# Performance work log

Measured on AMD Instinct MI355X. Metric: run time of the kernel, lower is better.

The kernel has to match this reference:

```python
import jax, jax.numpy as jnp
import numpy as np

K = 16  # knn_graph k, loop=True (self included since d(i,i)=0 is minimal)


def _knn_idx(pos, k):
    # exact kNN via pairwise squared distances; [N, k] neighbor indices
    sq = jnp.sum(pos * pos, axis=-1)
    d2 = sq[:, None] + sq[None, :] - 2.0 * (pos @ pos.T)  # [N, N]
    _, idx = jax.lax.top_k(-d2, k)
    return idx


def _pointnet_conv(x, pos, idx, Wa, ba, Wb, bb):
    # PointNetConv: msg = MLP(concat(x_j, pos_j - pos_i)), max-aggregate over neighbors
    rel = pos[idx] - pos[:, None, :]                    # [N, K, 3]
    m = jnp.concatenate([x[idx], rel], axis=-1)          # [N, K, Cin+3]
    h = jax.nn.relu(m @ Wa + ba) @ Wb + bb               # [N, K, Cout]
    return jnp.max(h, axis=1)                            # [N, Cout]


def setup_inputs() -> dict:
    key = jax.random.key(0)
    ks = jax.random.split(key, 13)
    N = 8192
    c1, c2, c3 = 64, 64, 128
    s = lambda fi: 1.0 / np.sqrt(fi)
    pos = jax.random.normal(ks[0], (N, 3), dtype=jnp.float32)
    return {
        "pos": pos,
        "W1a": jax.random.normal(ks[1], (3 + 3, c1), jnp.float32) * s(6),
        "b1a": jnp.zeros((c1,), jnp.float32),
        "W1b": jax.random.normal(ks[2], (c1, c1), jnp.float32) * s(c1),
        "b1b": jnp.zeros((c1,), jnp.float32),
        "W2a": jax.random.normal(ks[3], (c1 + 3, c2), jnp.float32) * s(c1 + 3),
        "b2a": jnp.zeros((c2,), jnp.float32),
        "W2b": jax.random.normal(ks[4], (c2, c2), jnp.float32) * s(c2),
        "b2b": jnp.zeros((c2,), jnp.float32),
        "W3a": jax.random.normal(ks[5], (c2 + 3, c3), jnp.float32) * s(c2 + 3),
        "b3a": jnp.zeros((c3,), jnp.float32),
        "W3b": jax.random.normal(ks[6], (c3, c3), jnp.float32) * s(c3),
        "b3b": jnp.zeros((c3,), jnp.float32),
    }


def reference(pos, W1a, b1a, W1b, b1b, W2a, b2a, W2b, b2b, W3a, b3a, W3b, b3b):
    idx = _knn_idx(pos, K)
    h1 = jax.nn.relu(_pointnet_conv(pos, pos, idx, W1a, b1a, W1b, b1b))
    h2 = jax.nn.relu(_pointnet_conv(h1, pos, idx, W2a, b2a, W2b, b2b))
    h3 = jax.nn.relu(_pointnet_conv(h2, pos, idx, W3a, b3a, W3b, b3b))
    return (h1, h2, h3)
```

## Files before the change

### kernel.cpp

```cpp
#include <hip/hip_runtime.h>
#include <math.h>

#define N_PTS 8192
#define KNN 16

typedef __attribute__((ext_vector_type(8))) short bf16x8;
typedef __attribute__((ext_vector_type(4))) float f32x4v;

__device__ __forceinline__ unsigned short f2bf(float f)
{
    unsigned u = __float_as_uint(f);
    u = u + 0x7fffu + ((u >> 16) & 1u);
    return (unsigned short)(u >> 16);
}
__device__ __forceinline__ unsigned pack2(float a, float b)
{
    return (unsigned)f2bf(a) | ((unsigned)f2bf(b) << 16);
}
__device__ __forceinline__ float rfl(float x)
{
    return __int_as_float(__builtin_amdgcn_readfirstlane(__float_as_int(x)));
}

__global__ __launch_bounds__(256) void prep_all(
    const float* __restrict__ pos, float4* __restrict__ pos4,
    const float* __restrict__ w1a, const float* __restrict__ w1b,
    const float* __restrict__ w2a, const float* __restrict__ w2b,
    const float* __restrict__ w3a, const float* __restrict__ w3b,
    uint4* __restrict__ dst)
{
    const int b = blockIdx.x;
    if (b < 88) {
        if (threadIdx.x >= 64) return;
        const float* Ws[6] = {w1a, w1b, w2a, w2b, w3a, w3b};
        const int Kd[6] = {6, 64, 67, 64, 67, 128};
        const int Nd[6] = {64, 64, 64, 64, 128, 128};
        const int start[7] = {0, 4, 12, 24, 32, 56, 88};
        int m = 0;
        while (b >= start[m + 1]) ++m;
        const int f  = b - start[m];
        const int NT = Nd[m] / 16;
        const int ks = f / NT, nt = f % NT;
        const int lane = threadIdx.x;
        const int c  = nt * 16 + (lane & 15);
        const int k0 = ks * 32 + (lane >> 4) * 8;
        const int K = Kd[m], N = Nd[m];
        const float* W = Ws[m];
        float v[8];
#pragma unroll
        for (int j = 0; j < 8; ++j) {
            const int kk = k0 + j;
            v[j] = (kk < K) ? W[kk * N + c] : 0.0f;
        }
        uint4 o;
        o.x = pack2(v[0], v[1]); o.y = pack2(v[2], v[3]);
        o.z = pack2(v[4], v[5]); o.w = pack2(v[6], v[7]);
        dst[b * 64 + lane] = o;
    } else {
        const int i = (b - 88) * 256 + threadIdx.x;
        const float x = pos[i * 3 + 0];
        const float y = pos[i * 3 + 1];
        const float z = pos[i * 3 + 2];
        pos4[i] = make_float4(x, y, z, fmaf(x, x, fmaf(y, y, z * z)));
    }
}

__device__ __forceinline__ unsigned sortkey(const float d2)
{
    unsigned u = __float_as_uint(d2);
    u ^= (unsigned)((int)u >> 31) | 0x80000000u;
    return u;
}

constexpr int CAP = 128;
constexpr int QB  = 8;
constexpr int NWV = 8;

__global__ __launch_bounds__(512, 8) void knn_kernel(const float4* __restrict__ pos4,
                                                     int* __restrict__ idx_out)
{
    __shared__ float mins[QB][NWV][64];
    __shared__ float Ts[QB];
    __shared__ unsigned long long surv[QB][CAP];
    __shared__ int scnt[QB];

    const int tid   = threadIdx.x;
    const int w     = tid >> 6;
    const int lane  = tid & 63;
    const int qbase = blockIdx.x * QB;
    const int cbase = w * (N_PTS / NWV);

    if (tid < QB) scnt[tid] = 0;

    float qx[QB], qy[QB], qz[QB];
#pragma unroll
    for (int qi = 0; qi < QB; ++qi) {
        const float4 qp = pos4[qbase + qi];
        qx[qi] = rfl(-2.0f * qp.x);
        qy[qi] = rfl(-2.0f * qp.y);
        qz[qi] = rfl(-2.0f * qp.z);
    }

    float mn[QB];
#pragma unroll
    for (int qi = 0; qi < QB; ++qi) mn[qi] = 1e30f;

    const float4* cp = pos4 + cbase + lane;

    {
        float4 c0 = cp[0 * 64], c1 = cp[1 * 64], c2 = cp[2 * 64], c3 = cp[3 * 64];
#pragma unroll 1
        for (int t = 0; t < 12; t += 4) {
            const float4 n0 = cp[(t + 4) * 64];
            const float4 n1 = cp[(t + 5) * 64];
            const float4 n2 = cp[(t + 6) * 64];
            const float4 n3 = cp[(t + 7) * 64];
#pragma unroll
            for (int qi = 0; qi < QB; ++qi) {
                mn[qi] = fminf(mn[qi], fmaf(qx[qi], c0.x, fmaf(qy[qi], c0.y, fmaf(qz[qi], c0.z, c0.w))));
                mn[qi] = fminf(mn[qi], fmaf(qx[qi], c1.x, fmaf(qy[qi], c1.y, fmaf(qz[qi], c1.z, c1.w))));
                mn[qi] = fminf(mn[qi], fmaf(qx[qi], c2.x, fmaf(qy[qi], c2.y, fmaf(qz[qi], c2.z, c2.w))));
                mn[qi] = fminf(mn[qi], fmaf(qx[qi], c3.x, fmaf(qy[qi], c3.y, fmaf(qz[qi], c3.z, c3.w))));
            }
            c0 = n0; c1 = n1; c2 = n2; c3 = n3;
        }
#pragma unroll
        for (int qi = 0; qi < QB; ++qi) {
            mn[qi] = fminf(mn[qi], fmaf(qx[qi], c0.x, fmaf(qy[qi], c0.y, fmaf(qz[qi], c0.z, c0.w))));
            mn[qi] = fminf(mn[qi], fmaf(qx[qi], c1.x, fmaf(qy[qi], c1.y, fmaf(qz[qi], c1.z, c1.w))));
            mn[qi] = fminf(mn[qi], fmaf(qx[qi], c2.x, fmaf(qy[qi], c2.y, fmaf(qz[qi], c2.z, c2.w))));
            mn[qi] = fminf(mn[qi], fmaf(qx[qi], c3.x, fmaf(qy[qi], c3.y, fmaf(qz[qi], c3.z, c3.w))));
        }
    }
#pragma unroll
    for (int qi = 0; qi < QB; ++qi) mins[qi][w][lane] = mn[qi];
    __syncthreads();

    {
        const int q = w;
        float v = mins[q][0][lane];
#pragma unroll
        for (int k = 1; k < NWV; ++k) v = fminf(v, mins[q][k][lane]);
#pragma unroll
        for (int kk = 2; kk <= 64; kk <<= 1)
#pragma unroll
            for (int j = kk >> 1; j > 0; j >>= 1) {
                const float o = __shfl_xor(v, j);
                const bool up = ((lane & kk) == 0);
                const bool lo = ((lane & j) == 0);
                v = (up == lo) ? fminf(v, o) : fmaxf(v, o);
            }
        if (lane == 15) Ts[q] = v;
    }
    __syncthreads();

    float T[QB];
#pragma unroll
    for (int qi = 0; qi < QB; ++qi) T[qi] = rfl(Ts[qi]);

    {
        float4 c0 = cp[0 * 64], c1 = cp[1 * 64], c2 = cp[2 * 64], c3 = cp[3 * 64];
#pragma unroll 1
        for (int t = 0; t < 16; t += 4) {
            float4 n0, n1, n2, n3;
            if (t < 12) {
                n0 = cp[(t + 4) * 64]; n1 = cp[(t + 5) * 64];
                n2 = cp[(t + 6) * 64]; n3 = cp[(t + 7) * 64];
            }
#pragma unroll
            for (int u = 0; u < 4; ++u) {
                const float4 p = (u == 0) ? c0 : (u == 1) ? c1 : (u == 2) ? c2 : c3;
                const int j = cbase + (t + u) * 64 + lane;
#pragma unroll
                for (int qi = 0; qi < QB; ++qi) {
                    const float s = fmaf(qx[qi], p.x, fmaf(qy[qi], p.y, fmaf(qz[qi], p.z, p.w)));
                    if (s <= T[qi]) {
                        const int slot = atomicAdd(&scnt[qi], 1);
                        if (slot < CAP)
                            surv[qi][slot] = ((unsigned long long)sortkey(s) << 32) | (unsigned)j;
                    }
                }
            }
            if (t < 12) { c0 = n0; c1 = n1; c2 = n2; c3 = n3; }
        }
    }
    __syncthreads();

    {
        const int q = w;
        const int n = min(scnt[q], CAP);
        const unsigned long long k0 = (lane < n) ? surv[q][lane] : ~0ull;
        const unsigned long long k1 = (lane + 64 < n) ? surv[q][lane + 64] : ~0ull;
        int r0 = 0, r1 = 0;
#pragma unroll 4
        for (int e = 0; e < n; ++e) {
            const unsigned long long ke = surv[q][e];
            r0 += (ke < k0) ? 1 : 0;
            r1 += (ke < k1) ? 1 : 0;
        }
        if (lane < n && r0 < KNN)
            idx_out[(qbase + q) * KNN + r0] = (int)(unsigned)(k0 & 0xFFFFFFFFu);
        if (lane + 64 < n && r1 < KNN)
            idx_out[(qbase + q) * KNN + r1] = (int)(unsigned)(k1 & 0xFFFFFFFFu);
    }
}

template <int CIN, int CMID, int COUT, int WM, int WN>
__global__ __launch_bounds__(256) void conv_mfma(
    const float* __restrict__ x, const float* __restrict__ pos,
    const int* __restrict__ idx,
    const uint4* __restrict__ fA, const float* __restrict__ ba,
    const uint4* __restrict__ fB, const float* __restrict__ bb,
    float* __restrict__ out)
{
    constexpr int PB  = 8, M = 128;
    constexpr int K1  = (CIN + 3 + 31) & ~31;
    constexpr int KS1 = K1 / 32;
    constexpr int KP1 = K1 + 8;
    constexpr int KS2 = CMID / 32;
    constexpr int KP2 = CMID + 8;
    constexpr int NT  = COUT / 16;
    constexpr int NTW = NT / WN;
    constexpr int MFW = (M / 16) / WM;
    constexpr int MSGS = M * KP1;
    constexpr int HBS  = M * KP2;
    constexpr int BUFS = (MSGS > HBS) ? MSGS : HBS;

    __shared__ int nbr[M];
    __shared__ __align__(16) unsigned short buf[BUFS];

    const int tid  = threadIdx.x;
    const int lane = tid & 63;
    const int w    = tid >> 6;
    const int wm   = w / WN, wn = w % WN;
    const int i0   = blockIdx.x * PB;

    if (tid < M) nbr[tid] = idx[i0 * KNN + tid];
    __syncthreads();

    if constexpr (CIN == 3) {
        if (tid < M) {
            const int row = tid, p = row >> 4, j = nbr[row];
            const float ax = pos[j * 3 + 0], ay = pos[j * 3 + 1], az = pos[j * 3 + 2];
            const float bx = pos[(i0 + p) * 3 + 0], by = pos[(i0 + p) * 3 + 1],
                        bz = pos[(i0 + p) * 3 + 2];
            uint4 c0;
            c0.x = pack2(ax, ay);
            c0.y = pack2(az, ax - bx);
            c0.z = pack2(ay - by, az - bz);
            c0.w = 0u;
            *reinterpret_cast<uint4*>(&buf[row * KP1 + 0])  = c0;
            const uint4 z = make_uint4(0, 0, 0, 0);
            *reinterpret_cast<uint4*>(&buf[row * KP1 + 8])  = z;
            *reinterpret_cast<uint4*>(&buf[row * KP1 + 16]) = z;
            *reinterpret_cast<uint4*>(&buf[row * KP1 + 24]) = z;
        }
    } else {
        const int row = tid >> 1, hh = tid & 1;
        const int j = nbr[row];
        const float* xr = x + j * CIN + hh * 32;
#pragma unroll
        for (int cc = 0; cc < 32; cc += 8) {
            const float4 f0 = *reinterpret_cast<const float4*>(xr + cc);
            const float4 f1 = *reinterpret_cast<const float4*>(xr + cc + 4);
            uint4 o;
            o.x = pack2(f0.x, f0.y); o.y = pack2(f0.z, f0.w);
            o.z = pack2(f1.x, f1.y); o.w = pack2(f1.z, f1.w);
            *reinterpret_cast<uint4*>(&buf[row * KP1 + hh * 32 + cc]) = o;
        }
        if (hh) {
            const int p = row >> 4;
            const float rx = pos[j * 3 + 0] - pos[(i0 + p) * 3 + 0];
            const float ry = pos[j * 3 + 1] - pos[(i0 + p) * 3 + 1];
            const float rz = pos[j * 3 + 2] - pos[(i0 + p) * 3 + 2];
            uint4 c0;
            c0.x = pack2(rx, ry);
            c0.y = pack2(rz, 0.0f);
            c0.z = 0u; c0.w = 0u;
            *reinterpret_cast<uint4*>(&buf[row * KP1 + 64]) = c0;
            const uint4 z = make_uint4(0, 0, 0, 0);
            *reinterpret_cast<uint4*>(&buf[row * KP1 + 72]) = z;
            *reinterpret_cast<uint4*>(&buf[row * KP1 + 80]) = z;
            *reinterpret_cast<uint4*>(&buf[row * KP1 + 88]) = z;
        }
    }
    __syncthreads();

    f32x4v acc[MFW][NTW];
    {
        uint4 b1[KS1][NTW];
#pragma unroll
        for (int ks = 0; ks < KS1; ++ks)
#pragma unroll
            for (int nt = 0; nt < NTW; ++nt)
                b1[ks][nt] = fA[(ks * NT + wn * NTW + nt) * 64 + lane];

#pragma unroll
        for (int mf = 0; mf < MFW; ++mf)
#pragma unroll
            for (int nt = 0; nt < NTW; ++nt) acc[mf][nt] = (f32x4v)0.0f;

#pragma unroll
        for (int mf = 0; mf < MFW; ++mf) {
            bf16x8 a[KS1];
#pragma unroll
            for (int ks = 0; ks < KS1; ++ks)
                a[ks] = *reinterpret_cast<const bf16x8*>(
                    &buf[((wm * MFW + mf) * 16 + (lane & 15)) * KP1 + ks * 32 + (lane >> 4) * 8]);
#pragma unroll
            for (int nt = 0; nt < NTW; ++nt)
#pragma unroll
                for (int ks = 0; ks < KS1; ++ks)
                    acc[mf][nt] = __builtin_amdgcn_mfma_f32_16x16x32_bf16(
                        a[ks], __builtin_bit_cast(bf16x8, b1[ks][nt]), acc[mf][nt], 0, 0, 0);
        }
    }
    __syncthreads();

    {
        float bav[NTW];
#pragma unroll
        for (int nt = 0; nt < NTW; ++nt) bav[nt] = ba[(wn * NTW + nt) * 16 + (lane & 15)];
#pragma unroll
        for (int mf = 0; mf < MFW; ++mf)
#pragma unroll
            for (int nt = 0; nt < NTW; ++nt)
#pragma unroll
                for (int r = 0; r < 4; ++r) {
                    const float v = fmaxf(acc[mf][nt][r] + bav[nt], 0.0f);
                    buf[((wm * MFW + mf) * 16 + (lane >> 4) * 4 + r) * KP2 +
                        (wn * NTW + nt) * 16 + (lane & 15)] = f2bf(v);
                }
    }
    __syncthreads();

    {
        uint4 b2[KS2][NTW];
#pragma unroll
        for (int ks = 0; ks < KS2; ++ks)
#pragma unroll
            for (int nt = 0; nt < NTW; ++nt)
                b2[ks][nt] = fB[(ks * NT + wn * NTW + nt) * 64 + lane];

        f32x4v acc2[MFW][NTW];
#pragma unroll
        for (int mf = 0; mf < MFW; ++mf)
#pragma unroll
            for (int nt = 0; nt < NTW; ++nt) acc2[mf][nt] = (f32x4v)0.0f;

#pragma unroll
        for (int mf = 0; mf < MFW; ++mf) {
            bf16x8 a[KS2];
#pragma unroll
            for (int ks = 0; ks < KS2; ++ks)
                a[ks] = *reinterpret_cast<const bf16x8*>(
                    &buf[((wm * MFW + mf) * 16 + (lane & 15)) * KP2 + ks * 32 + (lane >> 4) * 8]);
#pragma unroll
            for (int nt = 0; nt < NTW; ++nt)
#pragma unroll
                for (int ks = 0; ks < KS2; ++ks)
                    acc2[mf][nt] = __builtin_amdgcn_mfma_f32_16x16x32_bf16(
                        a[ks], __builtin_bit_cast(bf16x8, b2[ks][nt]), acc2[mf][nt], 0, 0, 0);
        }

        float bbv[NTW];
#pragma unroll
        for (int nt = 0; nt < NTW; ++nt) bbv[nt] = bb[(wn * NTW + nt) * 16 + (lane & 15)];

#pragma unroll
        for (int mf = 0; mf < MFW; ++mf)
#pragma unroll
            for (int nt = 0; nt < NTW; ++nt) {
                const f32x4v t = acc2[mf][nt];
                float m0 = fmaxf(fmaxf(t[0], t[1]), fmaxf(t[2], t[3]));
                m0 = fmaxf(m0, __shfl_xor(m0, 16));
                m0 = fmaxf(m0, __shfl_xor(m0, 32));
                const float v = fmaxf(m0 + bbv[nt], 0.0f);
                if (lane < 16)
                    out[(i0 + wm * MFW + mf) * COUT + (wn * NTW + nt) * 16 + lane] = v;
            }
    }
}

extern "C" void kernel_launch(void* const* d_in, const int* in_sizes, int n_in,
                              void* d_out, int out_size, void* d_ws, size_t ws_size,
                              hipStream_t stream)
{
    const float* pos = (const float*)d_in[0];
    const float* W1a = (const float*)d_in[1];
    const float* b1a = (const float*)d_in[2];
    const float* W1b = (const float*)d_in[3];
    const float* b1b = (const float*)d_in[4];
    const float* W2a = (const float*)d_in[5];
    const float* b2a = (const float*)d_in[6];
    const float* W2b = (const float*)d_in[7];
    const float* b2b = (const float*)d_in[8];
    const float* W3a = (const float*)d_in[9];
    const float* b3a = (const float*)d_in[10];
    const float* W3b = (const float*)d_in[11];
    const float* b3b = (const float*)d_in[12];

    float* out = (float*)d_out;
    float* h1 = out;
    float* h2 = out + N_PTS * 64;
    float* h3 = out + N_PTS * 128;

    int*   idx     = (int*)d_ws;
    uint4* wsFrags = (uint4*)((char*)d_ws + N_PTS * KNN * 4);

    float4* pos4 = (float4*)h3;

    prep_all<<<120, 256, 0, stream>>>(pos, pos4, W1a, W1b, W2a, W2b, W3a, W3b, wsFrags);
    knn_kernel<<<N_PTS / QB, 512, 0, stream>>>(pos4, idx);

    const uint4* fW1a = wsFrags + 0 * 64;
    const uint4* fW1b = wsFrags + 4 * 64;
    const uint4* fW2a = wsFrags + 12 * 64;
    const uint4* fW2b = wsFrags + 24 * 64;
    const uint4* fW3a = wsFrags + 32 * 64;
    const uint4* fW3b = wsFrags + 56 * 64;

    conv_mfma<3, 64, 64, 4, 1><<<N_PTS / 8, 256, 0, stream>>>(
        pos, pos, idx, fW1a, b1a, fW1b, b1b, h1);
    conv_mfma<64, 64, 64, 4, 1><<<N_PTS / 8, 256, 0, stream>>>(
        h1, pos, idx, fW2a, b2a, fW2b, b2b, h2);
    conv_mfma<64, 128, 128, 2, 2><<<N_PTS / 8, 256, 0, stream>>>(
        h2, pos, idx, fW3a, b3a, fW3b, b3b, h3);
}
```

Before: 82.39 us.

## Stage kNN candidate tiles into LDS via async global_load_lds double buffering

Replaces the per-wave register prefetch of candidate points in both kNN passes with double-buffered LDS tiles filled by global_load_lds, adding a block barrier per tile. It also stores the per-lane partial minima as round-up bf16 to shrink that shared array. The goal is to hide global load latency. The cost is 16 barriers per pass and less unrolling, and the bf16 rounding loosens the threshold, which may admit more survivors toward CAP.

```diff
diff --git a/kernel.cpp b/kernel.cpp
--- a/kernel.cpp
+++ b/kernel.cpp
@@ -20,6 +20,15 @@
 __device__ __forceinline__ float rfl(float x)
 {
     return __int_as_float(__builtin_amdgcn_readfirstlane(__float_as_int(x)));
+}
+__device__ __forceinline__ unsigned short bfup(float f)
+{
+    const unsigned u = __float_as_uint(f);
+    return (unsigned short)((u >> 31) ? (u >> 16) : ((u + 0xFFFFu) >> 16));
+}
+__device__ __forceinline__ float bfex(unsigned short h)
+{
+    return __uint_as_float((unsigned)h << 16);
 }
 
 __global__ __launch_bounds__(256) void prep_all(
@@ -72,14 +81,24 @@
     return u;
 }
 
-constexpr int CAP = 128;
-constexpr int QB  = 8;
-constexpr int NWV = 8;
+constexpr int CAP   = 128;
+constexpr int QB    = 8;
+constexpr int NWV   = 8;
+constexpr int TILE  = 512;
+constexpr int NTL   = N_PTS / TILE;
+
+__device__ __forceinline__ void stage_tile(const float4* src, float4* dst)
+{
+    __builtin_amdgcn_global_load_lds(
+        (const __attribute__((address_space(1))) void*)src,
+        (__attribute__((address_space(3))) void*)dst, 16, 0, 0);
+}
 
 __global__ __launch_bounds__(512, 8) void knn_kernel(const float4* __restrict__ pos4,
                                                      int* __restrict__ idx_out)
 {
-    __shared__ float mins[QB][NWV][64];
+    __shared__ float4 tile[2][TILE];
+    __shared__ unsigned short minsbf[QB][NWV][64];
     __shared__ float Ts[QB];
     __shared__ unsigned long long surv[QB][CAP];
     __shared__ int scnt[QB];
@@ -88,7 +107,6 @@
     const int w     = tid >> 6;
     const int lane  = tid & 63;
     const int qbase = blockIdx.x * QB;
-    const int cbase = w * (N_PTS / NWV);
 
     if (tid < QB) scnt[tid] = 0;
 
@@ -101,46 +119,35 @@
         qz[qi] = rfl(-2.0f * qp.z);
     }
 
+    const float4* src = pos4 + w * 64 + lane;
+
     float mn[QB];
 #pragma unroll
     for (int qi = 0; qi < QB; ++qi) mn[qi] = 1e30f;
 
-    const float4* cp = pos4 + cbase + lane;
-
-    {
-        float4 c0 = cp[0 * 64], c1 = cp[1 * 64], c2 = cp[2 * 64], c3 = cp[3 * 64];
+    stage_tile(src, &tile[0][w * 64]);
+    __syncthreads();
 #pragma unroll 1
-        for (int t = 0; t < 12; t += 4) {
-            const float4 n0 = cp[(t + 4) * 64];
-            const float4 n1 = cp[(t + 5) * 64];
-            const float4 n2 = cp[(t + 6) * 64];
-            const float4 n3 = cp[(t + 7) * 64];
-#pragma unroll
-            for (int qi = 0; qi < QB; ++qi) {
-                mn[qi] = fminf(mn[qi], fmaf(qx[qi], c0.x, fmaf(qy[qi], c0.y, fmaf(qz[qi], c0.z, c0.w))));
-                mn[qi] = fminf(mn[qi], fmaf(qx[qi], c1.x, fmaf(qy[qi], c1.y, fmaf(qz[qi], c1.z, c1.w))));
-                mn[qi] = fminf(mn[qi], fmaf(qx[qi], c2.x, fmaf(qy[qi], c2.y, fmaf(qz[qi], c2.z, c2.w))));
-                mn[qi] = fminf(mn[qi], fmaf(qx[qi], c3.x, fmaf(qy[qi], c3.y, fmaf(qz[qi], c3.z, c3.w))));
-            }
-            c0 = n0; c1 = n1; c2 = n2; c3 = n3;
-        }
+    for (int t = 0; t < NTL; ++t) {
+        if (t + 1 < NTL)
+            stage_tile(src + (t + 1) * TILE, &tile[(t + 1) & 1][w * 64]);
+        const float4 p = tile[t & 1][w * 64 + lane];
 #pragma unroll
         for (int qi = 0; qi < QB; ++qi) {
-            mn[qi] = fminf(mn[qi], fmaf(qx[qi], c0.x, fmaf(qy[qi], c0.y, fmaf(qz[qi], c0.z, c0.w))));
-            mn[qi] = fminf(mn[qi], fmaf(qx[qi], c1.x, fmaf(qy[qi], c1.y, fmaf(qz[qi], c1.z, c1.w))));
-            mn[qi] = fminf(mn[qi], fmaf(qx[qi], c2.x, fmaf(qy[qi], c2.y, fmaf(qz[qi], c2.z, c2.w))));
-            mn[qi] = fminf(mn[qi], fmaf(qx[qi], c3.x, fmaf(qy[qi], c3.y, fmaf(qz[qi], c3.z, c3.w))));
-        }
-    }
-#pragma unroll
-    for (int qi = 0; qi < QB; ++qi) mins[qi][w][lane] = mn[qi];
+            const float s = fmaf(qx[qi], p.x, fmaf(qy[qi], p.y, fmaf(qz[qi], p.z, p.w)));
+            mn[qi] = fminf(mn[qi], s);
+        }
+        __syncthreads();
+    }
+#pragma unroll
+    for (int qi = 0; qi < QB; ++qi) minsbf[qi][w][lane] = bfup(mn[qi]);
     __syncthreads();
 
     {
         const int q = w;
-        float v = mins[q][0][lane];
-#pragma unroll
-        for (int k = 1; k < NWV; ++k) v = fminf(v, mins[q][k][lane]);
+        float v = bfex(minsbf[q][0][lane]);
+#pragma unroll
+        for (int k = 1; k < NWV; ++k) v = fminf(v, bfex(minsbf[q][k][lane]));
 #pragma unroll
         for (int kk = 2; kk <= 64; kk <<= 1)
 #pragma unroll
@@ -158,33 +165,25 @@
 #pragma unroll
     for (int qi = 0; qi < QB; ++qi) T[qi] = rfl(Ts[qi]);
 
-    {
-        float4 c0 = cp[0 * 64], c1 = cp[1 * 64], c2 = cp[2 * 64], c3 = cp[3 * 64];
+    stage_tile(src, &tile[0][w * 64]);
+    __syncthreads();
 #pragma unroll 1
-        for (int t = 0; t < 16; t += 4) {
-            float4 n0, n1, n2, n3;
-            if (t < 12) {
-                n0 = cp[(t + 4) * 64]; n1 = cp[(t + 5) * 64];
-                n2 = cp[(t + 6) * 64]; n3 = cp[(t + 7) * 64];
+    for (int t = 0; t < NTL; ++t) {
+        if (t + 1 < NTL)
+            stage_tile(src + (t + 1) * TILE, &tile[(t + 1) & 1][w * 64]);
+        const float4 p = tile[t & 1][w * 64 + lane];
+        const int j = t * TILE + w * 64 + lane;
+#pragma unroll
+        for (int qi = 0; qi < QB; ++qi) {
+            const float s = fmaf(qx[qi], p.x, fmaf(qy[qi], p.y, fmaf(qz[qi], p.z, p.w)));
+            if (s <= T[qi]) {
+                const int slot = atomicAdd(&scnt[qi], 1);
+                if (slot < CAP)
+                    surv[qi][slot] = ((unsigned long long)sortkey(s) << 32) | (unsigned)j;
             }
-#pragma unroll
-            for (int u = 0; u < 4; ++u) {
-                const float4 p = (u == 0) ? c0 : (u == 1) ? c1 : (u == 2) ? c2 : c3;
-                const int j = cbase + (t + u) * 64 + lane;
-#pragma unroll
-                for (int qi = 0; qi < QB; ++qi) {
-                    const float s = fmaf(qx[qi], p.x, fmaf(qy[qi], p.y, fmaf(qz[qi], p.z, p.w)));
-                    if (s <= T[qi]) {
-                        const int slot = atomicAdd(&scnt[qi], 1);
-                        if (slot < CAP)
-                            surv[qi][slot] = ((unsigned long long)sortkey(s) << 32) | (unsigned)j;
-                    }
-                }
-            }
-            if (t < 12) { c0 = n0; c1 = n1; c2 = n2; c3 = n3; }
-        }
-    }
-    __syncthreads();
+        }
+        __syncthreads();
+    }
 
     {
         const int q = w;
```

Measured after the change: 76.93 us. -6.6%, faster.
